# Kernel optimization log

Measured on AMD Instinct MI355X. Metric: run time of the kernel, lower is better.

The kernel has to match this reference:

```python
import jax, jax.numpy as jnp
import numpy as np

H, L, S, D, NH, NKV, SL = 2048, 16, 2048, 128, 32, 8, 32768
T = S + L
REP = NH // NKV
HALF = D // 2
EPS = 1e-6
SCALE = D ** -0.5


def _rope_tables(positions):
    inv_freq = 1.0 / (10000.0 ** (jnp.arange(HALF, dtype=jnp.float32) / HALF))
    ang = positions[:, None].astype(jnp.float32) * inv_freq[None, :]  # (P, HALF)
    ang = jnp.concatenate([ang, ang], axis=-1)  # (P, D)
    return jnp.cos(ang), jnp.sin(ang)


def setup_inputs() -> dict:
    key = jax.random.key(0)
    ks = jax.random.split(key, 8)
    pos0 = 4096
    cos_q, sin_q = _rope_tables(jnp.arange(pos0 + S, pos0 + S + L))
    cos_k, sin_k = _rope_tables(jnp.arange(pos0, pos0 + T))
    return {
        'x': jax.random.normal(ks[0], (1, L, H), jnp.float32) * 0.02,
        'x_ctx': jax.random.normal(ks[1], (1, S, H), jnp.float32) * 0.02,
        'cos_q': cos_q, 'sin_q': sin_q, 'cos_k': cos_k, 'sin_k': sin_k,
        'kv_cache': jax.random.normal(ks[2], (2, NKV, SL, D), jnp.float32) * 0.02,
        'causal_mask': jnp.zeros((1, 1, L, SL), jnp.float32),
        'wq': jax.random.normal(ks[3], (NH * D, H), jnp.float32) * 0.02,
        'wk': jax.random.normal(ks[4], (NKV * D, H), jnp.float32) * 0.02,
        'wv': jax.random.normal(ks[5], (NKV * D, H), jnp.float32) * 0.02,
        'wo': jax.random.normal(ks[6], (H, NH * D), jnp.float32) * 0.02,
        'qn_w': jnp.ones((D,), jnp.float32),
        'kn_w': jnp.ones((D,), jnp.float32),
        'current_pos': 4096,
    }


def _ln_nobias(x, w):
    # 'ane' RMSNormSwitchable: x - mean, then layer_norm(weight, no bias) == LayerNorm
    m = jnp.mean(x, axis=-1, keepdims=True)
    xc = x - m
    var = jnp.mean(xc * xc, axis=-1, keepdims=True)
    return xc * jax.lax.rsqrt(var + EPS) * w


def _rope(x, cos, sin):
    x1, x2 = x[..., :HALF], x[..., HALF:]
    rot = jnp.concatenate([-x2, x1], axis=-1)
    return x * cos + rot * sin


def reference(x, x_ctx, cos_q, sin_q, cos_k, sin_k, kv_cache, causal_mask,
              wq, wk, wv, wo, qn_w, kn_w, current_pos):
    c = jnp.concatenate([x_ctx, x], axis=1)  # (1, T, H)
    q = (x @ wq.T).reshape(1, L, NH, D)
    k = (c @ wk.T).reshape(1, T, NKV, D)
    v = (c @ wv.T).reshape(1, T, NKV, D)
    q = jnp.transpose(_ln_nobias(q, qn_w), (0, 2, 1, 3))   # (1, NH, L, D)
    k = jnp.transpose(_ln_nobias(k, kn_w), (0, 2, 1, 3))   # (1, NKV, T, D)
    v = jnp.transpose(v, (0, 2, 1, 3))                      # (1, NKV, T, D)
    q = _rope(q, cos_q, sin_q)
    k = _rope(k, cos_k, sin_k)
    # in-place cache write (layer_idx = 0 -> slots 0 and 1)
    kv_cache = jax.lax.dynamic_update_slice(kv_cache, k, (0, 0, current_pos, 0))
    kv_cache = jax.lax.dynamic_update_slice(kv_cache, v, (1, 0, current_pos, 0))
    k_full = kv_cache[0]  # (NKV, SL, D)
    v_full = kv_cache[1]
    # GQA SDPA without materializing expanded K/V
    qg = q.reshape(1, NKV, REP, L, D)
    scores = jnp.einsum('bkrld,ksd->bkrls', qg, k_full) * SCALE
    scores = scores + causal_mask[:, :, None, :, :]  # (1,1,1,L,SL) broadcast
    attn = jax.nn.softmax(scores, axis=-1)
    out = jnp.einsum('bkrls,ksd->bkrld', attn, v_full).reshape(1, NH, L, D)
    out = jnp.transpose(out, (0, 2, 1, 3)).reshape(1, L, NH * D)
    return out @ wo.T, kv_cache
```

## Files before the change

### kernel.cpp

```cpp
#include <hip/hip_runtime.h>
#include <hip/hip_bf16.h>
#include <stdint.h>

#define H 2048
#define L 16
#define D 128
#define NH 32
#define NKV 8
#define SL 32768
#define T_TOT 2064
#define EPS 1e-6f
#define SCALE 0.08838834764831845f
#define NCHUNK 96

typedef __bf16 bf16x8 __attribute__((ext_vector_type(8)));
typedef float f32x4 __attribute__((ext_vector_type(4)));

__device__ __forceinline__ float bf2f(unsigned short u) {
  union { uint32_t i; float f; } v; v.i = ((uint32_t)u) << 16; return v.f;
}
__device__ __forceinline__ unsigned short f2bf(float f) {
  union { float f; uint32_t i; } v; v.f = f;
  uint32_t u = v.i;
  return (unsigned short)((u + 0x7FFFu + ((u >> 16) & 1u)) >> 16);
}
__device__ __forceinline__ void ld8f(const float* p, float* o) {
  float4 a = *(const float4*)p;
  float4 b = *(const float4*)(p + 4);
  o[0]=a.x; o[1]=a.y; o[2]=a.z; o[3]=a.w;
  o[4]=b.x; o[5]=b.y; o[6]=b.z; o[7]=b.w;
}
__device__ __forceinline__ void st8lds(unsigned short* d, const float* v) {
  unsigned short t[8];
#pragma unroll
  for (int j = 0; j < 8; ++j) t[j] = f2bf(v[j]);
  *(uint4*)d = *(const uint4*)t;
}
__device__ __forceinline__ void gl_lds16(const void* g, void* l) {
  __builtin_amdgcn_global_load_lds(
      (const __attribute__((address_space(1))) void*)g,
      (__attribute__((address_space(3))) void*)l, 16, 0, 0);
}

__global__ void k_conv(const float* __restrict__ wq, const float* __restrict__ wk,
                       const float* __restrict__ wv, const float* __restrict__ wo,
                       const float* __restrict__ x_ctx, const float* __restrict__ x,
                       unsigned short* __restrict__ wq_bf, unsigned short* __restrict__ wk_bf,
                       unsigned short* __restrict__ wv_bf, unsigned short* __restrict__ wo_bf,
                       unsigned short* __restrict__ xc_bf) {
  size_t li = (size_t)blockIdx.x * 256 + threadIdx.x;
  const float* src; unsigned short* dst;
  if (li < 1048576) { src = wq; dst = wq_bf; }
  else if ((li -= 1048576) < 262144) { src = wk; dst = wk_bf; }
  else if ((li -= 262144) < 262144) { src = wv; dst = wv_bf; }
  else if ((li -= 262144) < 1048576) { src = wo; dst = wo_bf; }
  else if ((li -= 1048576) < 524288) { src = x_ctx; dst = xc_bf; }
  else if ((li -= 524288) < 4096) { src = x; dst = xc_bf + (size_t)2048 * H; }
  else return;
  float v8[8];
  ld8f(src + li * 8, v8);
  unsigned short t[8];
#pragma unroll
  for (int j = 0; j < 8; ++j) t[j] = f2bf(v8[j]);
  *(uint4*)(dst + li * 8) = *(const uint4*)t;
}

__launch_bounds__(256)
__global__ void k_q_proj(const unsigned short* __restrict__ xq_bf,
                         const unsigned short* __restrict__ wq_bf,
                         float* __restrict__ qpart) {
  const int h = blockIdx.x, s = blockIdx.y;
  const int tid = threadIdx.x, lane = tid & 63, w = tid >> 6;
  __shared__ __align__(16) unsigned char Asm[2048];
  __shared__ __align__(16) unsigned char Bsm[16384];
  f32x4 zf = {0.f, 0.f, 0.f, 0.f};
  f32x4 acc[2] = {zf, zf};
  for (int kt = 0; kt < 2; ++kt) {
    if (w < 2) {
      int sl = w * 64 + lane;
      gl_lds16(xq_bf + (size_t)(sl >> 3) * H + s * 128 + kt * 64 + (sl & 7) * 8, Asm + w * 1024);
    }
#pragma unroll
    for (int q = 0; q < 4; ++q) {
      int sl = (w * 4 + q) * 64 + lane;
      gl_lds16(wq_bf + (size_t)(h * 128 + (sl >> 3)) * H + s * 128 + kt * 64 + (sl & 7) * 8,
               Bsm + (w * 4 + q) * 1024);
    }
    __syncthreads();
#pragma unroll
    for (int ks = 0; ks < 2; ++ks) {
      bf16x8 a = *(const bf16x8*)(Asm + (lane & 15) * 128 + ks * 64 + (lane >> 4) * 16);
#pragma unroll
      for (int j = 0; j < 2; ++j) {
        int nr = w * 32 + j * 16 + (lane & 15);
        bf16x8 b = *(const bf16x8*)(Bsm + nr * 128 + ks * 64 + (lane >> 4) * 16);
        acc[j] = __builtin_amdgcn_mfma_f32_16x16x32_bf16(a, b, acc[j], 0, 0, 0);
      }
    }
    __syncthreads();
  }
#pragma unroll
  for (int j = 0; j < 2; ++j)
#pragma unroll
    for (int e = 0; e < 4; ++e) {
      int lq = (lane >> 4) * 4 + e;
      int col = w * 32 + j * 16 + (lane & 15);
      qpart[((size_t)(s * NH + h) * L + lq) * D + col] = acc[j][e];
    }
}

__global__ void k_q_fin(const float* __restrict__ qpart, const float* __restrict__ qn_w,
                        const float* __restrict__ cos_q, const float* __restrict__ sin_q,
                        unsigned short* __restrict__ qbf) {
  const int head = blockIdx.x >> 4;
  const int l = blockIdx.x & 15;
  const int d = threadIdx.x;
  __shared__ float ybuf[128];
  __shared__ float red[4];
  float v = 0;
  for (int s = 0; s < 16; ++s) v += qpart[((size_t)(s * NH + head) * L + l) * D + d];
  float s1 = v, s2 = v * v;
  for (int m = 1; m < 64; m <<= 1) { s1 += __shfl_xor(s1, m); s2 += __shfl_xor(s2, m); }
  if ((threadIdx.x & 63) == 0) { red[(threadIdx.x >> 6) * 2] = s1; red[(threadIdx.x >> 6) * 2 + 1] = s2; }
  __syncthreads();
  float sum = red[0] + red[2], sumsq = red[1] + red[3];
  float mean = sum * (1.0f / 128.0f);
  float var = sumsq * (1.0f / 128.0f) - mean * mean;
  float rs = rsqrtf(fmaxf(var, 0.f) + EPS);
  float z = (v - mean) * rs * qn_w[d];
  ybuf[d] = z;
  __syncthreads();
  float zp = ybuf[d ^ 64];
  float rot = (d < 64) ? -zp : zp;
  float o = z * cos_q[l * D + d] + rot * sin_q[l * D + d];
  qbf[(size_t)(head * L + l) * D + d] = f2bf(o);
}

__launch_bounds__(256)
__global__ void k_kv_gemm(const unsigned short* __restrict__ xc_bf,
                          const unsigned short* __restrict__ wk_bf,
                          const unsigned short* __restrict__ wv_bf,
                          const float* __restrict__ kn_w,
                          const float* __restrict__ cos_k, const float* __restrict__ sin_k,
                          const int* __restrict__ cur_pos, float* __restrict__ cache) {
  const int bn = blockIdx.x;
  const int bm = blockIdx.y;
  const int tid = threadIdx.x, lane = tid & 63, wid = tid >> 6;
  const int wm = wid >> 1, wn = wid & 1;

  __shared__ __align__(16) unsigned char smem[36864];
  unsigned char* A = smem;
  unsigned char* B = smem + 16384;

  const unsigned short* wsrc = (bn < 8) ? wk_bf + (size_t)(bn * 128) * H
                                        : wv_bf + (size_t)((bn - 8) * 128) * H;
  int arow[4], brow[4], c8[4];
#pragma unroll
  for (int q = 0; q < 4; ++q) {
    int sl = (wid * 4 + q) * 64 + lane;
    brow[q] = sl >> 3;
    c8[q] = (sl & 7) * 8;
    int t = bm * 128 + brow[q]; if (t > 2063) t = 2063;
    arow[q] = t;
  }

  f32x4 acc[4][4];
  f32x4 zf = {0.f, 0.f, 0.f, 0.f};
#pragma unroll
  for (int i = 0; i < 4; ++i)
#pragma unroll
    for (int j = 0; j < 4; ++j) acc[i][j] = zf;

  for (int kt = 0; kt < H / 64; ++kt) {
#pragma unroll
    for (int q = 0; q < 4; ++q)
      gl_lds16(xc_bf + (size_t)arow[q] * H + kt * 64 + c8[q], A + (wid * 4 + q) * 1024);
#pragma unroll
    for (int q = 0; q < 4; ++q)
      gl_lds16(wsrc + (size_t)brow[q] * H + kt * 64 + c8[q], B + (wid * 4 + q) * 1024);
    __syncthreads();
#pragma unroll
    for (int ks = 0; ks < 2; ++ks) {
      bf16x8 a[4], b[4];
#pragma unroll
      for (int i = 0; i < 4; ++i) {
        int row = wm * 64 + i * 16 + (lane & 15);
        a[i] = *(const bf16x8*)(A + row * 128 + ks * 64 + (lane >> 4) * 16);
      }
#pragma unroll
      for (int j = 0; j < 4; ++j) {
        int nr = wn * 64 + j * 16 + (lane & 15);
        b[j] = *(const bf16x8*)(B + nr * 128 + ks * 64 + (lane >> 4) * 16);
      }
#pragma unroll
      for (int i = 0; i < 4; ++i)
#pragma unroll
        for (int j = 0; j < 4; ++j)
          acc[i][j] = __builtin_amdgcn_mfma_f32_16x16x32_bf16(a[i], b[j], acc[i][j], 0, 0, 0);
    }
    __syncthreads();
  }

  float* cs = (float*)smem;
  float* lnp = (float*)(smem + 33024);
  const int pos0 = *cur_pos;
  for (int half = 0; half < 2; ++half) {
    __syncthreads();
    if (wm == half) {
#pragma unroll
      for (int i = 0; i < 4; ++i)
#pragma unroll
        for (int j = 0; j < 4; ++j)
#pragma unroll
          for (int e = 0; e < 4; ++e) {
            int r = i * 16 + (lane >> 4) * 4 + e;
            int c = wn * 64 + j * 16 + (lane & 15);
            cs[r * 129 + c] = acc[i][j][e];
          }
    }
    __syncthreads();
    if (bn < 8 && tid < 64) {
      int r = tid;
      float sum = 0, sumsq = 0;
      for (int d2 = 0; d2 < 128; ++d2) { float v = cs[r * 129 + d2]; sum += v; sumsq += v * v; }
      float mean = sum * (1.0f / 128.0f);
      float var = sumsq * (1.0f / 128.0f) - mean * mean;
      lnp[r * 2] = mean;
      lnp[r * 2 + 1] = rsqrtf(fmaxf(var, 0.f) + EPS);
    }
    __syncthreads();
    {
      int r = tid >> 2, q = tid & 3;
      int t = bm * 128 + half * 64 + r;
      if (t < T_TOT) {
        if (bn < 8) {
          float mean = lnp[r * 2], rs = lnp[r * 2 + 1];
          float* dst = cache + ((size_t)bn * SL + (size_t)(pos0 + t)) * D;
#pragma unroll
          for (int i8 = 0; i8 < 8; ++i8) {
            int d2 = q * 32 + i8 * 4;
            float4 o4;
            float* o = (float*)&o4;
#pragma unroll
            for (int e = 0; e < 4; ++e) {
              int dd = d2 + e;
              float z = (cs[r * 129 + dd] - mean) * rs * kn_w[dd];
              int p = dd ^ 64;
              float zp = (cs[r * 129 + p] - mean) * rs * kn_w[p];
              float rot = (dd < 64) ? -zp : zp;
              o[e] = z * cos_k[(size_t)t * D + dd] + rot * sin_k[(size_t)t * D + dd];
            }
            *(float4*)(dst + d2) = o4;
          }
        } else {
          float* dst = cache + ((size_t)(NKV + (bn - 8)) * SL + (size_t)(pos0 + t)) * D;
#pragma unroll
          for (int i8 = 0; i8 < 8; ++i8) {
            int d2 = q * 32 + i8 * 4;
            float4 o4 = { cs[r * 129 + d2], cs[r * 129 + d2 + 1], cs[r * 129 + d2 + 2], cs[r * 129 + d2 + 3] };
            *(float4*)(dst + d2) = o4;
          }
        }
      }
    }
  }
}

__launch_bounds__(256)
__global__ void k_attn(const float* __restrict__ kv_src, float* __restrict__ cache,
                       const unsigned short* __restrict__ qbf, const float* __restrict__ mask,
                       const int* __restrict__ cur_pos,
                       unsigned short* __restrict__ part_O,
                       float* __restrict__ part_m, float* __restrict__ part_l) {
  const int g = blockIdx.x;
  const int ch = blockIdx.y;
  const int tid = threadIdx.x, lane = tid & 63, w = tid >> 6;
  const int t0 = ch * 5 + (ch < 32 ? ch : 32);
  const int t1 = t0 + 5 + (ch < 32 ? 1 : 0);
  const int pos0 = *cur_pos, pos1 = pos0 + T_TOT;

  __shared__ __align__(16) unsigned short Klds[64 * 136];
  __shared__ __align__(16) unsigned short Vt[128 * 72];
  __shared__ __align__(16) unsigned short Plds[4 * 16 * 72];

  bf16x8 qf[4];
#pragma unroll
  for (int ks = 0; ks < 4; ++ks)
    qf[ks] = *(const bf16x8*)(qbf + ((size_t)(g * 4 + w) * L + (lane & 15)) * D + ks * 32 + (lane >> 4) * 8);

  f32x4 O[8];
  f32x4 zf = {0.f, 0.f, 0.f, 0.f};
#pragma unroll
  for (int j = 0; j < 8; ++j) O[j] = zf;
  float mrow[4] = {-1e30f, -1e30f, -1e30f, -1e30f};
  float lrow[4] = {0, 0, 0, 0};
  unsigned short* Pw = Plds + w * 16 * 72;

  float4 ka[4], kb[4], va[4], vb[4];
  float mrgC[16], mrgN[16];
  int pp[4];

#define LOADT(ti_) do {                                                         \
    _Pragma("unroll")                                                           \
    for (int g2 = 0; g2 < 4; ++g2) {                                            \
      int slot = tid + g2 * 256;                                                \
      int pos = slot >> 4, c0 = (slot & 15) * 8;                                \
      int p = (ti_) * 64 + pos;                                                 \
      pp[g2] = p;                                                               \
      bool u = (p >= pos0) & (p < pos1);                                        \
      const float* sp = u ? cache : kv_src;                                     \
      size_t kidx = ((size_t)g * SL + p) * D + c0;                              \
      size_t vidx = ((size_t)(NKV + g) * SL + p) * D + c0;                      \
      ka[g2] = *(const float4*)(sp + kidx);                                     \
      kb[g2] = *(const float4*)(sp + kidx + 4);                                 \
      va[g2] = *(const float4*)(sp + vidx);                                     \
      vb[g2] = *(const float4*)(sp + vidx + 4);                                 \
    }                                                                           \
    _Pragma("unroll")                                                           \
    for (int ee = 0; ee < 4; ++ee)                                              \
      _Pragma("unroll")                                                         \
      for (int nf2 = 0; nf2 < 4; ++nf2)                                         \
        mrgN[ee * 4 + nf2] = mask[(size_t)((lane >> 4) * 4 + ee) * SL +         \
                                  (ti_) * 64 + nf2 * 16 + (lane & 15)];         \
  } while (0)

#define WRITET() do {                                                           \
    _Pragma("unroll")                                                           \
    for (int g2 = 0; g2 < 4; ++g2) {                                            \
      int slot = tid + g2 * 256;                                                \
      int pos = slot >> 4, c0 = (slot & 15) * 8;                                \
      int p = pp[g2];                                                           \
      bool u = (p >= pos0) & (p < pos1);                                        \
      if (!u) {                                                                 \
        size_t kidx = ((size_t)g * SL + p) * D + c0;                            \
        size_t vidx = ((size_t)(NKV + g) * SL + p) * D + c0;                    \
        *(float4*)(cache + kidx) = ka[g2];                                      \
        *(float4*)(cache + kidx + 4) = kb[g2];                                  \
        *(float4*)(cache + vidx) = va[g2];                                      \
        *(float4*)(cache + vidx + 4) = vb[g2];                                  \
      }                                                                         \
      float kf[8] = {ka[g2].x, ka[g2].y, ka[g2].z, ka[g2].w,                    \
                     kb[g2].x, kb[g2].y, kb[g2].z, kb[g2].w};                   \
      st8lds(Klds + pos * 136 + c0, kf);                                        \
      float vf[8] = {va[g2].x, va[g2].y, va[g2].z, va[g2].w,                    \
                     vb[g2].x, vb[g2].y, vb[g2].z, vb[g2].w};                   \
      _Pragma("unroll")                                                         \
      for (int jj = 0; jj < 8; ++jj) {                                          \
        int dd = c0 + jj;                                                       \
        Vt[dd * 72 + (pos ^ (((dd >> 3) & 7) << 3))] = f2bf(vf[jj]);            \
      }                                                                         \
    }                                                                           \
  } while (0)

  LOADT(t0);
  for (int ti = t0; ti < t1; ++ti) {
    WRITET();
#pragma unroll
    for (int ii = 0; ii < 16; ++ii) mrgC[ii] = mrgN[ii];
    if (ti + 1 < t1) LOADT(ti + 1);
    __syncthreads();

    f32x4 Sv[4];
#pragma unroll
    for (int nf = 0; nf < 4; ++nf) {
      f32x4 accs = zf;
#pragma unroll
      for (int ks = 0; ks < 4; ++ks) {
        int pl = nf * 16 + (lane & 15);
        bf16x8 bk = *(const bf16x8*)(Klds + pl * 136 + ks * 32 + (lane >> 4) * 8);
        accs = __builtin_amdgcn_mfma_f32_16x16x32_bf16(qf[ks], bk, accs, 0, 0, 0);
      }
      Sv[nf] = accs;
    }

#pragma unroll
    for (int e = 0; e < 4; ++e) {
      int lq = (lane >> 4) * 4 + e;
      float sc[4];
#pragma unroll
      for (int nf = 0; nf < 4; ++nf)
        sc[nf] = Sv[nf][e] * SCALE + mrgC[e * 4 + nf];
      float tmax = fmaxf(fmaxf(sc[0], sc[1]), fmaxf(sc[2], sc[3]));
#pragma unroll
      for (int mm = 1; mm < 16; mm <<= 1) tmax = fmaxf(tmax, __shfl_xor(tmax, mm));
      float mnew = fmaxf(mrow[e], tmax);
      float alpha = __expf(mrow[e] - mnew);
      float psum = 0;
#pragma unroll
      for (int nf = 0; nf < 4; ++nf) {
        float p = __expf(sc[nf] - mnew);
        psum += p;
        Pw[lq * 72 + nf * 16 + (lane & 15)] = f2bf(p);
      }
#pragma unroll
      for (int mm = 1; mm < 16; mm <<= 1) psum += __shfl_xor(psum, mm);
      lrow[e] = lrow[e] * alpha + psum;
      mrow[e] = mnew;
#pragma unroll
      for (int j = 0; j < 8; ++j) O[j][e] *= alpha;
    }

#pragma unroll
    for (int ks2 = 0; ks2 < 2; ++ks2) {
      bf16x8 ap = *(const bf16x8*)(Pw + (lane & 15) * 72 + ks2 * 32 + (lane >> 4) * 8);
#pragma unroll
      for (int jf = 0; jf < 8; ++jf) {
        int dd = jf * 16 + (lane & 15);
        int po = (ks2 * 32 + (lane >> 4) * 8) ^ (((dd >> 3) & 7) << 3);
        bf16x8 bv = *(const bf16x8*)(Vt + dd * 72 + po);
        O[jf] = __builtin_amdgcn_mfma_f32_16x16x32_bf16(ap, bv, O[jf], 0, 0, 0);
      }
    }
    __syncthreads();
  }
#undef LOADT
#undef WRITET

  const int cidx = g * NCHUNK + ch;
#pragma unroll
  for (int jf = 0; jf < 8; ++jf)
#pragma unroll
    for (int e = 0; e < 4; ++e) {
      int qr = w * 16 + (lane >> 4) * 4 + e;
      part_O[((size_t)cidx * 64 + qr) * D + jf * 16 + (lane & 15)] = f2bf(O[jf][e]);
    }
  if ((lane & 15) == 0) {
#pragma unroll
    for (int e = 0; e < 4; ++e) {
      int qr = w * 16 + (lane >> 4) * 4 + e;
      part_m[cidx * 64 + qr] = mrow[e];
      part_l[cidx * 64 + qr] = lrow[e];
    }
  }
}

__global__ void k_attn_reduce(const unsigned short* __restrict__ part_O,
                              const float* __restrict__ part_m,
                              const float* __restrict__ part_l,
                              unsigned short* __restrict__ attnbf) {
  const int g = blockIdx.x >> 6;
  const int qr = blockIdx.x & 63;
  const int d = threadIdx.x;
  float M = -1e30f;
  for (int c = 0; c < NCHUNK; ++c) M = fmaxf(M, part_m[(g * NCHUNK + c) * 64 + qr]);
  float Lsum = 0, acc = 0;
  for (int c = 0; c < NCHUNK; ++c) {
    float wgt = __expf(part_m[(g * NCHUNK + c) * 64 + qr] - M);
    Lsum += part_l[(g * NCHUNK + c) * 64 + qr] * wgt;
    acc += wgt * bf2f(part_O[((size_t)(g * NCHUNK + c) * 64 + qr) * D + d]);
  }
  float o = acc / fmaxf(Lsum, 1e-20f);
  int h = g * 4 + (qr >> 4), l = qr & 15;
  attnbf[(size_t)l * 4096 + h * 128 + d] = f2bf(o);
}

__launch_bounds__(256)
__global__ void k_out_gemm(const unsigned short* __restrict__ attnbf,
                           const unsigned short* __restrict__ wo_bf,
                           float* __restrict__ part_out) {
  const int ntile = blockIdx.x;
  const int ksp = blockIdx.y;
  const int tid = threadIdx.x, lane = tid & 63, w = tid >> 6;
  __shared__ __align__(16) unsigned char Asm[2048];
  __shared__ __align__(16) unsigned char Bsm[16384];

  f32x4 zf = {0.f, 0.f, 0.f, 0.f};
  f32x4 acc[2] = {zf, zf};
  for (int it = 0; it < 4; ++it) {
    if (w < 2) {
      int sl = w * 64 + lane;
      gl_lds16(attnbf + (size_t)(sl >> 3) * 4096 + ksp * 256 + it * 64 + (sl & 7) * 8, Asm + w * 1024);
    }
#pragma unroll
    for (int q = 0; q < 4; ++q) {
      int sl = (w * 4 + q) * 64 + lane;
      gl_lds16(wo_bf + (size_t)(ntile * 128 + (sl >> 3)) * 4096 + ksp * 256 + it * 64 + (sl & 7) * 8,
               Bsm + (w * 4 + q) * 1024);
    }
    __syncthreads();
#pragma unroll
    for (int ks = 0; ks < 2; ++ks) {
      bf16x8 a = *(const bf16x8*)(Asm + (lane & 15) * 128 + ks * 64 + (lane >> 4) * 16);
#pragma unroll
      for (int j = 0; j < 2; ++j) {
        int nr = w * 32 + j * 16 + (lane & 15);
        bf16x8 b = *(const bf16x8*)(Bsm + nr * 128 + ks * 64 + (lane >> 4) * 16);
        acc[j] = __builtin_amdgcn_mfma_f32_16x16x32_bf16(a, b, acc[j], 0, 0, 0);
      }
    }
    __syncthreads();
  }
#pragma unroll
  for (int j = 0; j < 2; ++j)
#pragma unroll
    for (int e = 0; e < 4; ++e) {
      int lq = (lane >> 4) * 4 + e;
      int n = ntile * 128 + w * 32 + j * 16 + (lane & 15);
      part_out[(size_t)ksp * 32768 + lq * 2048 + n] = acc[j][e];
    }
}

__global__ void k_out_combine(const float* __restrict__ part_out, float* __restrict__ out0) {
  int i = blockIdx.x * 256 + threadIdx.x;
  if (i < 32768) {
    float v = 0;
    for (int c = 0; c < 16; ++c) v += part_out[c * 32768 + i];
    out0[i] = v;
  }
}

extern "C" void kernel_launch(void* const* d_in, const int* in_sizes, int n_in,
                              void* d_out, int out_size, void* d_ws, size_t ws_size,
                              hipStream_t stream) {
  const float* x     = (const float*)d_in[0];
  const float* x_ctx = (const float*)d_in[1];
  const float* cos_q = (const float*)d_in[2];
  const float* sin_q = (const float*)d_in[3];
  const float* cos_k = (const float*)d_in[4];
  const float* sin_k = (const float*)d_in[5];
  const float* kv    = (const float*)d_in[6];
  const float* mask  = (const float*)d_in[7];
  const float* wq    = (const float*)d_in[8];
  const float* wk    = (const float*)d_in[9];
  const float* wv    = (const float*)d_in[10];
  const float* wo    = (const float*)d_in[11];
  const float* qn_w  = (const float*)d_in[12];
  const float* kn_w  = (const float*)d_in[13];
  const int* cur_pos = (const int*)d_in[14];

  float* out0 = (float*)d_out;
  float* cache = out0 + 32768;

  uint8_t* ws = (uint8_t*)d_ws;
  unsigned short* xc_bf  = (unsigned short*)(ws);
  unsigned short* wq_bf  = (unsigned short*)(ws + 0x0810000);
  unsigned short* wk_bf  = (unsigned short*)(ws + 0x1810000);
  unsigned short* wv_bf  = (unsigned short*)(ws + 0x1C10000);
  unsigned short* wo_bf  = (unsigned short*)(ws + 0x2010000);
  float* qpart           = (float*)(ws + 0x3010000);
  unsigned short* qbf    = (unsigned short*)(ws + 0x3410000);
  unsigned short* attnbf = (unsigned short*)(ws + 0x3430000);
  unsigned short* part_O = (unsigned short*)(ws + 0x3450000);
  float* part_m          = (float*)(ws + 0x4050000);
  float* part_l          = (float*)(ws + 0x4090000);
  float* part_out        = (float*)(ws + 0x40D0000);

  unsigned short* xq_bf = xc_bf + (size_t)2048 * H;

  k_conv<<<dim3(12304), dim3(256), 0, stream>>>(wq, wk, wv, wo, x_ctx, x,
                                                wq_bf, wk_bf, wv_bf, wo_bf, xc_bf);
  k_q_proj<<<dim3(32, 16), dim3(256), 0, stream>>>(xq_bf, wq_bf, qpart);
  k_q_fin<<<dim3(512), dim3(128), 0, stream>>>(qpart, qn_w, cos_q, sin_q, qbf);
  k_kv_gemm<<<dim3(16, 17), dim3(256), 0, stream>>>(xc_bf, wk_bf, wv_bf, kn_w, cos_k, sin_k, cur_pos, cache);
  k_attn<<<dim3(8, NCHUNK), dim3(256), 0, stream>>>(kv, cache, qbf, mask, cur_pos, part_O, part_m, part_l);
  k_attn_reduce<<<dim3(512), dim3(128), 0, stream>>>(part_O, part_m, part_l, attnbf);
  k_out_gemm<<<dim3(16, 16), dim3(256), 0, stream>>>(attnbf, wo_bf, part_out);
  k_out_combine<<<dim3(128), dim3(256), 0, stream>>>(part_out, out0);
}
```

Before: 264.4 us.

## Convert wq/wo to bf16 inside GEMMs, shrink KV GEMM tile, nontemporal cache streaming

Drops the separate fp32-to-bf16 conversion pass for wq and wo. The Q-projection and output GEMMs now load fp32 weights directly and convert them while staging into LDS. This removes a full write and re-read of those weights, at the cost of loading twice as many bytes per tile through plain loads instead of direct-to-LDS loads. The KV GEMM M-tile is halved to 64 rows, doubling the grid and removing the two-pass epilogue. Attention cache reads and writes use nontemporal loads and stores to avoid polluting the cache.

```diff
diff --git a/kernel.cpp b/kernel.cpp
--- a/kernel.cpp
+++ b/kernel.cpp
@@ -42,19 +42,15 @@
       (__attribute__((address_space(3))) void*)l, 16, 0, 0);
 }
 
-__global__ void k_conv(const float* __restrict__ wq, const float* __restrict__ wk,
-                       const float* __restrict__ wv, const float* __restrict__ wo,
+__global__ void k_conv(const float* __restrict__ wk, const float* __restrict__ wv,
                        const float* __restrict__ x_ctx, const float* __restrict__ x,
-                       unsigned short* __restrict__ wq_bf, unsigned short* __restrict__ wk_bf,
-                       unsigned short* __restrict__ wv_bf, unsigned short* __restrict__ wo_bf,
+                       unsigned short* __restrict__ wk_bf, unsigned short* __restrict__ wv_bf,
                        unsigned short* __restrict__ xc_bf) {
   size_t li = (size_t)blockIdx.x * 256 + threadIdx.x;
   const float* src; unsigned short* dst;
-  if (li < 1048576) { src = wq; dst = wq_bf; }
-  else if ((li -= 1048576) < 262144) { src = wk; dst = wk_bf; }
+  if (li < 262144) { src = wk; dst = wk_bf; }
   else if ((li -= 262144) < 262144) { src = wv; dst = wv_bf; }
-  else if ((li -= 262144) < 1048576) { src = wo; dst = wo_bf; }
-  else if ((li -= 1048576) < 524288) { src = x_ctx; dst = xc_bf; }
+  else if ((li -= 262144) < 524288) { src = x_ctx; dst = xc_bf; }
   else if ((li -= 524288) < 4096) { src = x; dst = xc_bf + (size_t)2048 * H; }
   else return;
   float v8[8];
@@ -67,7 +63,7 @@
 
 __launch_bounds__(256)
 __global__ void k_q_proj(const unsigned short* __restrict__ xq_bf,
-                         const unsigned short* __restrict__ wq_bf,
+                         const float* __restrict__ wq,
                          float* __restrict__ qpart) {
   const int h = blockIdx.x, s = blockIdx.y;
   const int tid = threadIdx.x, lane = tid & 63, w = tid >> 6;
@@ -83,8 +79,10 @@
 #pragma unroll
     for (int q = 0; q < 4; ++q) {
       int sl = (w * 4 + q) * 64 + lane;
-      gl_lds16(wq_bf + (size_t)(h * 128 + (sl >> 3)) * H + s * 128 + kt * 64 + (sl & 7) * 8,
-               Bsm + (w * 4 + q) * 1024);
+      int row = sl >> 3, c0 = (sl & 7) * 8;
+      float v8[8];
+      ld8f(wq + (size_t)(h * 128 + row) * H + s * 128 + kt * 64 + c0, v8);
+      st8lds((unsigned short*)Bsm + row * 64 + c0, v8);
     }
     __syncthreads();
 #pragma unroll
@@ -148,43 +146,46 @@
   const int tid = threadIdx.x, lane = tid & 63, wid = tid >> 6;
   const int wm = wid >> 1, wn = wid & 1;
 
-  __shared__ __align__(16) unsigned char smem[36864];
+  __shared__ __align__(16) unsigned char smem[33536];
   unsigned char* A = smem;
-  unsigned char* B = smem + 16384;
+  unsigned char* B = smem + 8192;
 
   const unsigned short* wsrc = (bn < 8) ? wk_bf + (size_t)(bn * 128) * H
                                         : wv_bf + (size_t)((bn - 8) * 128) * H;
-  int arow[4], brow[4], c8[4];
+  int arow[2], ac8[2], brow[4], bc8[4];
+#pragma unroll
+  for (int q = 0; q < 2; ++q) {
+    int sl = (wid * 2 + q) * 64 + lane;
+    int t = bm * 64 + (sl >> 3); if (t > 2063) t = 2063;
+    arow[q] = t; ac8[q] = (sl & 7) * 8;
+  }
 #pragma unroll
   for (int q = 0; q < 4; ++q) {
     int sl = (wid * 4 + q) * 64 + lane;
-    brow[q] = sl >> 3;
-    c8[q] = (sl & 7) * 8;
-    int t = bm * 128 + brow[q]; if (t > 2063) t = 2063;
-    arow[q] = t;
-  }
-
-  f32x4 acc[4][4];
+    brow[q] = sl >> 3; bc8[q] = (sl & 7) * 8;
+  }
+
+  f32x4 acc[2][4];
   f32x4 zf = {0.f, 0.f, 0.f, 0.f};
 #pragma unroll
-  for (int i = 0; i < 4; ++i)
+  for (int i = 0; i < 2; ++i)
 #pragma unroll
     for (int j = 0; j < 4; ++j) acc[i][j] = zf;
 
   for (int kt = 0; kt < H / 64; ++kt) {
 #pragma unroll
+    for (int q = 0; q < 2; ++q)
+      gl_lds16(xc_bf + (size_t)arow[q] * H + kt * 64 + ac8[q], A + (wid * 2 + q) * 1024);
+#pragma unroll
     for (int q = 0; q < 4; ++q)
-      gl_lds16(xc_bf + (size_t)arow[q] * H + kt * 64 + c8[q], A + (wid * 4 + q) * 1024);
-#pragma unroll
-    for (int q = 0; q < 4; ++q)
-      gl_lds16(wsrc + (size_t)brow[q] * H + kt * 64 + c8[q], B + (wid * 4 + q) * 1024);
+      gl_lds16(wsrc + (size_t)brow[q] * H + kt * 64 + bc8[q], B + (wid * 4 + q) * 1024);
     __syncthreads();
 #pragma unroll
     for (int ks = 0; ks < 2; ++ks) {
-      bf16x8 a[4], b[4];
-#pragma unroll
-      for (int i = 0; i < 4; ++i) {
-        int row = wm * 64 + i * 16 + (lane & 15);
+      bf16x8 a[2], b[4];
+#pragma unroll
+      for (int i = 0; i < 2; ++i) {
+        int row = wm * 32 + i * 16 + (lane & 15);
         a[i] = *(const bf16x8*)(A + row * 128 + ks * 64 + (lane >> 4) * 16);
       }
 #pragma unroll
@@ -193,7 +194,7 @@
         b[j] = *(const bf16x8*)(B + nr * 128 + ks * 64 + (lane >> 4) * 16);
       }
 #pragma unroll
-      for (int i = 0; i < 4; ++i)
+      for (int i = 0; i < 2; ++i)
 #pragma unroll
         for (int j = 0; j < 4; ++j)
           acc[i][j] = __builtin_amdgcn_mfma_f32_16x16x32_bf16(a[i], b[j], acc[i][j], 0, 0, 0);
@@ -204,62 +205,57 @@
   float* cs = (float*)smem;
   float* lnp = (float*)(smem + 33024);
   const int pos0 = *cur_pos;
-  for (int half = 0; half < 2; ++half) {
-    __syncthreads();
-    if (wm == half) {
-#pragma unroll
-      for (int i = 0; i < 4; ++i)
-#pragma unroll
-        for (int j = 0; j < 4; ++j)
+#pragma unroll
+  for (int i = 0; i < 2; ++i)
+#pragma unroll
+    for (int j = 0; j < 4; ++j)
+#pragma unroll
+      for (int e = 0; e < 4; ++e) {
+        int r = wm * 32 + i * 16 + (lane >> 4) * 4 + e;
+        int c = wn * 64 + j * 16 + (lane & 15);
+        cs[r * 129 + c] = acc[i][j][e];
+      }
+  __syncthreads();
+  if (bn < 8 && tid < 64) {
+    int r = tid;
+    float sum = 0, sumsq = 0;
+    for (int d2 = 0; d2 < 128; ++d2) { float v = cs[r * 129 + d2]; sum += v; sumsq += v * v; }
+    float mean = sum * (1.0f / 128.0f);
+    float var = sumsq * (1.0f / 128.0f) - mean * mean;
+    lnp[r * 2] = mean;
+    lnp[r * 2 + 1] = rsqrtf(fmaxf(var, 0.f) + EPS);
+  }
+  __syncthreads();
+  {
+    int r = tid >> 2, q = tid & 3;
+    int t = bm * 64 + r;
+    if (t < T_TOT) {
+      if (bn < 8) {
+        float mean = lnp[r * 2], rs = lnp[r * 2 + 1];
+        float* dst = cache + ((size_t)bn * SL + (size_t)(pos0 + t)) * D;
+#pragma unroll
+        for (int i8 = 0; i8 < 8; ++i8) {
+          int d2 = q * 32 + i8 * 4;
+          float4 o4;
+          float* o = (float*)&o4;
 #pragma unroll
           for (int e = 0; e < 4; ++e) {
-            int r = i * 16 + (lane >> 4) * 4 + e;
-            int c = wn * 64 + j * 16 + (lane & 15);
-            cs[r * 129 + c] = acc[i][j][e];
+            int dd = d2 + e;
+            float z = (cs[r * 129 + dd] - mean) * rs * kn_w[dd];
+            int p = dd ^ 64;
+            float zp = (cs[r * 129 + p] - mean) * rs * kn_w[p];
+            float rot = (dd < 64) ? -zp : zp;
+            o[e] = z * cos_k[(size_t)t * D + dd] + rot * sin_k[(size_t)t * D + dd];
           }
-    }
-    __syncthreads();
-    if (bn < 8 && tid < 64) {
-      int r = tid;
-      float sum = 0, sumsq = 0;
-      for (int d2 = 0; d2 < 128; ++d2) { float v = cs[r * 129 + d2]; sum += v; sumsq += v * v; }
-      float mean = sum * (1.0f / 128.0f);
-      float var = sumsq * (1.0f / 128.0f) - mean * mean;
-      lnp[r * 2] = mean;
-      lnp[r * 2 + 1] = rsqrtf(fmaxf(var, 0.f) + EPS);
-    }
-    __syncthreads();
-    {
-      int r = tid >> 2, q = tid & 3;
-      int t = bm * 128 + half * 64 + r;
-      if (t < T_TOT) {
-        if (bn < 8) {
-          float mean = lnp[r * 2], rs = lnp[r * 2 + 1];
-          float* dst = cache + ((size_t)bn * SL + (size_t)(pos0 + t)) * D;
-#pragma unroll
-          for (int i8 = 0; i8 < 8; ++i8) {
-            int d2 = q * 32 + i8 * 4;
-            float4 o4;
-            float* o = (float*)&o4;
-#pragma unroll
-            for (int e = 0; e < 4; ++e) {
-              int dd = d2 + e;
-              float z = (cs[r * 129 + dd] - mean) * rs * kn_w[dd];
-              int p = dd ^ 64;
-              float zp = (cs[r * 129 + p] - mean) * rs * kn_w[p];
-              float rot = (dd < 64) ? -zp : zp;
-              o[e] = z * cos_k[(size_t)t * D + dd] + rot * sin_k[(size_t)t * D + dd];
-            }
-            *(float4*)(dst + d2) = o4;
-          }
-        } else {
-          float* dst = cache + ((size_t)(NKV + (bn - 8)) * SL + (size_t)(pos0 + t)) * D;
-#pragma unroll
-          for (int i8 = 0; i8 < 8; ++i8) {
-            int d2 = q * 32 + i8 * 4;
-            float4 o4 = { cs[r * 129 + d2], cs[r * 129 + d2 + 1], cs[r * 129 + d2 + 2], cs[r * 129 + d2 + 3] };
-            *(float4*)(dst + d2) = o4;
-          }
+          *(float4*)(dst + d2) = o4;
+        }
+      } else {
+        float* dst = cache + ((size_t)(NKV + (bn - 8)) * SL + (size_t)(pos0 + t)) * D;
+#pragma unroll
+        for (int i8 = 0; i8 < 8; ++i8) {
+          int d2 = q * 32 + i8 * 4;
+          float4 o4 = { cs[r * 129 + d2], cs[r * 129 + d2 + 1], cs[r * 129 + d2 + 2], cs[r * 129 + d2 + 3] };
+          *(float4*)(dst + d2) = o4;
         }
       }
     }
@@ -296,7 +292,7 @@
   float lrow[4] = {0, 0, 0, 0};
   unsigned short* Pw = Plds + w * 16 * 72;
 
-  float4 ka[4], kb[4], va[4], vb[4];
+  f32x4 ka[4], kb[4], va[4], vb[4];
   float mrgC[16], mrgN[16];
   int pp[4];
 
@@ -311,10 +307,10 @@
       const float* sp = u ? cache : kv_src;                                     \
       size_t kidx = ((size_t)g * SL + p) * D + c0;                              \
       size_t vidx = ((size_t)(NKV + g) * SL + p) * D + c0;                      \
-      ka[g2] = *(const float4*)(sp + kidx);                                     \
-      kb[g2] = *(const float4*)(sp + kidx + 4);                                 \
-      va[g2] = *(const float4*)(sp + vidx);                                     \
-      vb[g2] = *(const float4*)(sp + vidx + 4);                                 \
+      ka[g2] = __builtin_nontemporal_load((const f32x4*)(sp + kidx));           \
+      kb[g2] = __builtin_nontemporal_load((const f32x4*)(sp + kidx + 4));       \
+      va[g2] = __builtin_nontemporal_load((const f32x4*)(sp + vidx));           \
+      vb[g2] = __builtin_nontemporal_load((const f32x4*)(sp + vidx + 4));       \
     }                                                                           \
     _Pragma("unroll")                                                           \
     for (int ee = 0; ee < 4; ++ee)                                              \
@@ -334,16 +330,16 @@
       if (!u) {                                                                 \
         size_t kidx = ((size_t)g * SL + p) * D + c0;                            \
         size_t vidx = ((size_t)(NKV + g) * SL + p) * D + c0;                    \
-        *(float4*)(cache + kidx) = ka[g2];                                      \
-        *(float4*)(cache + kidx + 4) = kb[g2];                                  \
-        *(float4*)(cache + vidx) = va[g2];                                      \
-        *(float4*)(cache + vidx + 4) = vb[g2];                                  \
+        __builtin_nontemporal_store(ka[g2], (f32x4*)(cache + kidx));            \
+        __builtin_nontemporal_store(kb[g2], (f32x4*)(cache + kidx + 4));        \
+        __builtin_nontemporal_store(va[g2], (f32x4*)(cache + vidx));            \
+        __builtin_nontemporal_store(vb[g2], (f32x4*)(cache + vidx + 4));        \
       }                                                                         \
-      float kf[8] = {ka[g2].x, ka[g2].y, ka[g2].z, ka[g2].w,                    \
-                     kb[g2].x, kb[g2].y, kb[g2].z, kb[g2].w};                   \
+      float kf[8] = {ka[g2][0], ka[g2][1], ka[g2][2], ka[g2][3],                \
+                     kb[g2][0], kb[g2][1], kb[g2][2], kb[g2][3]};               \
       st8lds(Klds + pos * 136 + c0, kf);                                        \
-      float vf[8] = {va[g2].x, va[g2].y, va[g2].z, va[g2].w,                    \
-                     vb[g2].x, vb[g2].y, vb[g2].z, vb[g2].w};                   \
+      float vf[8] = {va[g2][0], va[g2][1], va[g2][2], va[g2][3],                \
+                     vb[g2][0], vb[g2][1], vb[g2][2], vb[g2][3]};               \
       _Pragma("unroll")                                                         \
       for (int jj = 0; jj < 8; ++jj) {                                          \
         int dd = c0 + jj;                                                       \
@@ -456,7 +452,7 @@
 
 __launch_bounds__(256)
 __global__ void k_out_gemm(const unsigned short* __restrict__ attnbf,
-                           const unsigned short* __restrict__ wo_bf,
+                           const float* __restrict__ wo,
                            float* __restrict__ part_out) {
   const int ntile = blockIdx.x;
   const int ksp = blockIdx.y;
@@ -474,8 +470,10 @@
 #pragma unroll
     for (int q = 0; q < 4; ++q) {
       int sl = (w * 4 + q) * 64 + lane;
-      gl_lds16(wo_bf + (size_t)(ntile * 128 + (sl >> 3)) * 4096 + ksp * 256 + it * 64 + (sl & 7) * 8,
-               Bsm + (w * 4 + q) * 1024);
+      int row = sl >> 3, c0 = (sl & 7) * 8;
+      float v8[8];
+      ld8f(wo + (size_t)(ntile * 128 + row) * 4096 + ksp * 256 + it * 64 + c0, v8);
+      st8lds((unsigned short*)Bsm + row * 64 + c0, v8);
     }
     __syncthreads();
 #pragma unroll
@@ -533,27 +531,24 @@
 
   uint8_t* ws = (uint8_t*)d_ws;
   unsigned short* xc_bf  = (unsigned short*)(ws);
-  unsigned short* wq_bf  = (unsigned short*)(ws + 0x0810000);
-  unsigned short* wk_bf  = (unsigned short*)(ws + 0x1810000);
-  unsigned short* wv_bf  = (unsigned short*)(ws + 0x1C10000);
-  unsigned short* wo_bf  = (unsigned short*)(ws + 0x2010000);
-  float* qpart           = (float*)(ws + 0x3010000);
-  unsigned short* qbf    = (unsigned short*)(ws + 0x3410000);
-  unsigned short* attnbf = (unsigned short*)(ws + 0x3430000);
-  unsigned short* part_O = (unsigned short*)(ws + 0x3450000);
-  float* part_m          = (float*)(ws + 0x4050000);
-  float* part_l          = (float*)(ws + 0x4090000);
-  float* part_out        = (float*)(ws + 0x40D0000);
+  unsigned short* wk_bf  = (unsigned short*)(ws + 0x0810000);
+  unsigned short* wv_bf  = (unsigned short*)(ws + 0x0C10000);
+  float* qpart           = (float*)(ws + 0x1010000);
+  unsigned short* qbf    = (unsigned short*)(ws + 0x1410000);
+  unsigned short* attnbf = (unsigned short*)(ws + 0x1430000);
+  unsigned short* part_O = (unsigned short*)(ws + 0x1450000);
+  float* part_m          = (float*)(ws + 0x2050000);
+  float* part_l          = (float*)(ws + 0x2090000);
+  float* part_out        = (float*)(ws + 0x20D0000);
 
   unsigned short* xq_bf = xc_bf + (size_t)2048 * H;
 
-  k_conv<<<dim3(12304), dim3(256), 0, stream>>>(wq, wk, wv, wo, x_ctx, x,
-                                                wq_bf, wk_bf, wv_bf, wo_bf, xc_bf);
-  k_q_proj<<<dim3(32, 16), dim3(256), 0, stream>>>(xq_bf, wq_bf, qpart);
+  k_conv<<<dim3(4112), dim3(256), 0, stream>>>(wk, wv, x_ctx, x, wk_bf, wv_bf, xc_bf);
+  k_q_proj<<<dim3(32, 16), dim3(256), 0, stream>>>(xq_bf, wq, qpart);
   k_q_fin<<<dim3(512), dim3(128), 0, stream>>>(qpart, qn_w, cos_q, sin_q, qbf);
-  k_kv_gemm<<<dim3(16, 17), dim3(256), 0, stream>>>(xc_bf, wk_bf, wv_bf, kn_w, cos_k, sin_k, cur_pos, cache);
+  k_kv_gemm<<<dim3(16, 33), dim3(256), 0, stream>>>(xc_bf, wk_bf, wv_bf, kn_w, cos_k, sin_k, cur_pos, cache);
   k_attn<<<dim3(8, NCHUNK), dim3(256), 0, stream>>>(kv, cache, qbf, mask, cur_pos, part_O, part_m, part_l);
   k_attn_reduce<<<dim3(512), dim3(128), 0, stream>>>(part_O, part_m, part_l, attnbf);
-  k_out_gemm<<<dim3(16, 16), dim3(256), 0, stream>>>(attnbf, wo_bf, part_out);
+  k_out_gemm<<<dim3(16, 16), dim3(256), 0, stream>>>(attnbf, wo, part_out);
   k_out_combine<<<dim3(128), dim3(256), 0, stream>>>(part_out, out0);
 }
```

Result: slower. 279.7 us (+5.8%).
